# Kernel tuning notes

Hardware: AMD Instinct MI355X
Metric: run time of the kernel (lower is better)

## Reference

```python
import jax, jax.numpy as jnp
import numpy as np

D_MODEL = 1024
N_HEADS = 16
D_HEAD = D_MODEL // N_HEADS
L_NS = 64
B = 1
L_S_VAL = 4096


def setup_inputs() -> dict:
    key = jax.random.key(0)
    k0, k1, k2, k3 = jax.random.split(key, 4)
    d = D_MODEL
    x = jax.random.normal(k0, (B, L_S_VAL + L_NS, d), dtype=jnp.float32)
    # xavier-uniform-ish scales
    s_qkv = (2.0 / (d + 3 * d)) ** 0.5
    s_out = (2.0 / (d + d)) ** 0.5
    W_S = jax.random.normal(k1, (d, 3 * d), dtype=jnp.float32) * s_qkv
    W_NS = jax.random.normal(k2, (L_NS, d, 3 * d), dtype=jnp.float32) * s_qkv
    W_out = jax.random.normal(k3, (d, d), dtype=jnp.float32) * s_out
    return {"x": x, "W_S": W_S, "W_NS": W_NS, "W_out": W_out,
            "L_S": L_S_VAL, "query_start": 2048}


def reference(x, W_S, W_NS, W_out, L_S, query_start):
    Bsz, L_total, D = x.shape
    H, Dh = N_HEADS, D_HEAD
    L_q = L_S - query_start

    x_S = x[:, :L_S]                    # (B, L_S, D)
    x_NS = x[:, L_S:L_S + L_NS]         # (B, L_NS, D)

    qkv_S = jnp.einsum('bsd,do->bso', x_S, W_S)        # shared projection
    qkv_NS = jnp.einsum('bnd,ndo->bno', x_NS, W_NS)    # per-NS-token projection

    Q_S, K_S, V_S = jnp.split(qkv_S, 3, axis=-1)
    Q_NS, K_NS, V_NS = jnp.split(qkv_NS, 3, axis=-1)

    Q = jnp.concatenate([Q_S[:, query_start:], Q_NS], axis=1)  # (B, L_q+L_NS, D)
    K = jnp.concatenate([K_S, K_NS], axis=1)                    # (B, L_total, D)
    V = jnp.concatenate([V_S, V_NS], axis=1)

    def to_heads(t):
        return t.reshape(Bsz, t.shape[1], H, Dh).transpose(0, 2, 1, 3)

    Qh, Kh, Vh = to_heads(Q), to_heads(K), to_heads(V)

    q_pos = jnp.arange(query_start, L_S + L_NS)  # (L_q+L_NS,)
    k_pos = jnp.arange(L_total)                  # (L_total,)
    causal_mask = q_pos[:, None] < k_pos[None, :]  # True = masked out

    scale = Dh ** -0.5
    scores = jnp.einsum('bhqd,bhkd->bhqk', Qh, Kh) * scale
    scores = jnp.where(causal_mask[None, None], -jnp.inf, scores)
    attn = jax.nn.softmax(scores, axis=-1)
    attn = jnp.nan_to_num(attn)

    out = jnp.einsum('bhqk,bhkd->bhqd', attn, Vh)
    out = out.transpose(0, 2, 1, 3).reshape(Bsz, L_q + L_NS, D)
    return jnp.einsum('bqd,de->bqe', out, W_out)
```

## Files before the change

kernel.cpp:

```cpp
#include <hip/hip_runtime.h>

typedef __attribute__((ext_vector_type(8))) short bf16x8;
typedef __attribute__((ext_vector_type(4))) float f32x4;

#define MFMA_BF16(a,b,c) __builtin_amdgcn_mfma_f32_16x16x32_bf16(a,b,c,0,0,0)

#define H_ 16
#define DH 64
#define LQ 2112
#define LK 4160
#define QOFF 2048
#define DM 1024
#define NO 3072

__device__ __forceinline__ unsigned short f2bf(float f) {
  union { float f; unsigned u; } v; v.f = f;
  unsigned u = v.u;
  return (unsigned short)((u + 0x7FFFu + ((u >> 16) & 1u)) >> 16);
}

__device__ __forceinline__ void gl_lds16(const unsigned short* g, unsigned short* l) {
  __builtin_amdgcn_global_load_lds(
      (const __attribute__((address_space(1))) unsigned int*)g,
      (__attribute__((address_space(3))) unsigned int*)l,
      16, 0, 0);
}

__global__ __launch_bounds__(256) void cvt_x(const float* __restrict__ x,
                                             unsigned short* __restrict__ xb) {
  int i = blockIdx.x * 256 + threadIdx.x;
  float4 f = ((const float4*)x)[i];
  ushort4 o;
  o.x = f2bf(f.x); o.y = f2bf(f.y); o.z = f2bf(f.z); o.w = f2bf(f.w);
  ((ushort4*)xb)[i] = o;
}

__global__ __launch_bounds__(256) void transp_bf(const float* __restrict__ in,
                                                 unsigned short* __restrict__ out,
                                                 int R, int C) {
  __shared__ float t[32][33];
  int c0 = blockIdx.x * 32, r0 = blockIdx.y * 32;
  #pragma unroll
  for (int i = threadIdx.y; i < 32; i += 8)
    t[i][threadIdx.x] = in[(size_t)(r0 + i) * C + c0 + threadIdx.x];
  __syncthreads();
  #pragma unroll
  for (int i = threadIdx.y; i < 32; i += 8)
    out[(size_t)(c0 + i) * R + r0 + threadIdx.x] = f2bf(t[threadIdx.x][i]);
}

__global__ __launch_bounds__(256) void qkv_ns_k(const float* __restrict__ x,
                                                const float* __restrict__ W_NS,
                                                float* __restrict__ qkvNS) {
  int oc = blockIdx.x, dc = blockIdx.y, n = blockIdx.z;
  __shared__ float xs[256];
  xs[threadIdx.x] = x[(size_t)(4096 + n) * DM + dc * 256 + threadIdx.x];
  __syncthreads();
  int o0 = oc * 1024 + threadIdx.x * 4;
  const float* W = W_NS + ((size_t)n * DM + dc * 256) * NO + o0;
  float a0 = 0.f, a1 = 0.f, a2 = 0.f, a3 = 0.f;
  #pragma unroll 4
  for (int d = 0; d < 256; ++d) {
    float xv = xs[d];
    float4 w = *(const float4*)(W + (size_t)d * NO);
    a0 = fmaf(xv, w.x, a0); a1 = fmaf(xv, w.y, a1);
    a2 = fmaf(xv, w.z, a2); a3 = fmaf(xv, w.w, a3);
  }
  float* dst = qkvNS + (size_t)n * NO + o0;
  atomicAdd(dst + 0, a0); atomicAdd(dst + 1, a1);
  atomicAdd(dst + 2, a2); atomicAdd(dst + 3, a3);
}

__global__ __launch_bounds__(256) void scatter_ns(const float* __restrict__ qkvNS,
                                                  unsigned short* __restrict__ Qb,
                                                  unsigned short* __restrict__ Kb,
                                                  unsigned short* __restrict__ VbT) {
  int i = blockIdx.x * 256 + threadIdx.x;
  int n = i / NO, o = i - n * NO;
  float v = qkvNS[i];
  int h = (o & 1023) >> 6, dh = o & 63;
  if (o < 1024)       Qb[((size_t)h * LQ + 2048 + n) * DH + dh] = f2bf(v * 0.125f);
  else if (o < 2048)  Kb[((size_t)h * LK + 4096 + n) * DH + dh] = f2bf(v);
  else                VbT[((size_t)(h * 64 + dh)) * LK + 4096 + n] = f2bf(v);
}

__global__ __launch_bounds__(256) void gemm_qkv(const unsigned short* __restrict__ A,
                                                const unsigned short* __restrict__ BT,
                                                unsigned short* __restrict__ Qb,
                                                unsigned short* __restrict__ Kb,
                                                unsigned short* __restrict__ VbT) {
  __shared__ unsigned short At[128 * 32];
  __shared__ unsigned short Bt[128 * 32];
  int tm = blockIdx.x * 128, tn = blockIdx.y * 128;
  int tid = threadIdx.x, wave = tid >> 6, lane = tid & 63;
  int col = lane & 15, quad = lane >> 4;
  int wr = (wave & 1) * 64, wc = (wave >> 1) * 64;
  int srow = tid >> 2, spart = (tid & 3) * 8;

  f32x4 acc[4][4] = {};

  for (int kb = 0; kb < DM; kb += 32) {
    __syncthreads();
    gl_lds16(&A[(size_t)(tm + srow) * DM + kb + spart],       &At[wave * 512]);
    gl_lds16(&A[(size_t)(tm + srow + 64) * DM + kb + spart],  &At[2048 + wave * 512]);
    gl_lds16(&BT[(size_t)(tn + srow) * DM + kb + spart],      &Bt[wave * 512]);
    gl_lds16(&BT[(size_t)(tn + srow + 64) * DM + kb + spart], &Bt[2048 + wave * 512]);
    __syncthreads();
    bf16x8 af[4], bfr[4];
    #pragma unroll
    for (int i = 0; i < 4; ++i) {
      af[i]  = *(const bf16x8*)&At[(wr + i * 16 + col) * 32 + quad * 8];
      bfr[i] = *(const bf16x8*)&Bt[(wc + i * 16 + col) * 32 + quad * 8];
    }
    #pragma unroll
    for (int i = 0; i < 4; ++i)
      #pragma unroll
      for (int j = 0; j < 4; ++j)
        acc[i][j] = MFMA_BF16(af[i], bfr[j], acc[i][j]);
  }

  if (tn >= 2048) {
    #pragma unroll
    for (int i = 0; i < 4; ++i)
      #pragma unroll
      for (int j = 0; j < 4; ++j) {
        int n = tn + wc + j * 16 + col;
        int h = (n & 1023) >> 6, dh = n & 63;
        int m0 = tm + wr + i * 16 + quad * 4;
        ushort4 o;
        o.x = f2bf(acc[i][j][0]); o.y = f2bf(acc[i][j][1]);
        o.z = f2bf(acc[i][j][2]); o.w = f2bf(acc[i][j][3]);
        *(ushort4*)&VbT[((size_t)(h * 64 + dh)) * LK + m0] = o;
      }
  } else if (tn >= 1024) {
    #pragma unroll
    for (int i = 0; i < 4; ++i)
      #pragma unroll
      for (int j = 0; j < 4; ++j)
        #pragma unroll
        for (int r = 0; r < 4; ++r) {
          int m = tm + wr + i * 16 + quad * 4 + r;
          int n = tn + wc + j * 16 + col;
          int h = (n & 1023) >> 6, dh = n & 63;
          Kb[((size_t)h * LK + m) * DH + dh] = f2bf(acc[i][j][r]);
        }
  } else {
    #pragma unroll
    for (int i = 0; i < 4; ++i)
      #pragma unroll
      for (int j = 0; j < 4; ++j)
        #pragma unroll
        for (int r = 0; r < 4; ++r) {
          int m = tm + wr + i * 16 + quad * 4 + r;
          int n = tn + wc + j * 16 + col;
          int h = (n & 1023) >> 6, dh = n & 63;
          if (m >= QOFF) Qb[((size_t)h * LQ + (m - QOFF)) * DH + dh] = f2bf(acc[i][j][r] * 0.125f);
        }
  }
}

__global__ __launch_bounds__(256) void attn(const unsigned short* __restrict__ Qb,
                                            const unsigned short* __restrict__ Kb,
                                            const unsigned short* __restrict__ VbT,
                                            unsigned short* __restrict__ Ob) {
  __shared__ unsigned short Kt[2][64 * 64];
  __shared__ unsigned short Vt[2][64 * 64];
  __shared__ unsigned short Pt[4][16 * 72];
  int h = blockIdx.y;
  int qb = blockIdx.x * 64;
  int tid = threadIdx.x, wave = tid >> 6, lane = tid & 63;
  int col = lane & 15, quad = lane >> 4;
  const unsigned short* Qh = Qb + (size_t)h * LQ * DH;
  const unsigned short* Kh = Kb + (size_t)h * LK * DH;
  const unsigned short* Vh = VbT + (size_t)h * 64 * LK;

  int qrow = qb + wave * 16 + col;
  bf16x8 aq0 = *(const bf16x8*)&Qh[qrow * DH + quad * 8];
  bf16x8 aq1 = *(const bf16x8*)&Qh[qrow * DH + 32 + quad * 8];

  f32x4 oacc[4] = {};
  float m_i[4] = {-3e38f, -3e38f, -3e38f, -3e38f};
  float l_i[4] = {0.f, 0.f, 0.f, 0.f};

  int row0 = tid >> 3;
  int sc8  = ((tid & 7) ^ (row0 & 7)) * 8;
  int xs   = col & 7;

#define STAGE(b, kb_) do { \
    gl_lds16(&Kh[(size_t)((kb_) + row0) * DH + sc8],        &Kt[b][wave * 512]); \
    gl_lds16(&Kh[(size_t)((kb_) + row0 + 32) * DH + sc8],   &Kt[b][2048 + wave * 512]); \
    gl_lds16(&Vh[(size_t)row0 * LK + (kb_) + sc8],          &Vt[b][wave * 512]); \
    gl_lds16(&Vh[(size_t)(row0 + 32) * LK + (kb_) + sc8],   &Vt[b][2048 + wave * 512]); \
  } while (0)

  int nkt = 33 + blockIdx.x;
  STAGE(0, 0);
  int cur = 0;
  for (int kt = 0; kt < nkt; ++kt) {
    int kb = kt << 6;
    __syncthreads();
    if (kt + 1 < nkt) STAGE(cur ^ 1, (kt + 1) << 6);

    const unsigned short* K_ = Kt[cur];
    const unsigned short* V_ = Vt[cur];

    f32x4 s[4] = {};
    #pragma unroll
    for (int f = 0; f < 4; ++f) {
      int krow = (f * 16 + col) * 64;
      bf16x8 b0 = *(const bf16x8*)&K_[krow + (quad ^ xs) * 8];
      bf16x8 b1 = *(const bf16x8*)&K_[krow + (((4 + quad) ^ xs)) * 8];
      s[f] = MFMA_BF16(aq0, b0, s[f]);
      s[f] = MFMA_BF16(aq1, b1, s[f]);
    }

    float alpha[4];
    bool lastt = (kt == nkt - 1);
    #pragma unroll
    for (int r = 0; r < 4; ++r) {
      float v0 = s[0][r], v1 = s[1][r], v2 = s[2][r], v3 = s[3][r];
      if (lastt) {
        int kmax = QOFF + qb + wave * 16 + quad * 4 + r;
        v0 = (kb + col      <= kmax) ? v0 : -3e38f;
        v1 = (kb + 16 + col <= kmax) ? v1 : -3e38f;
        v2 = (kb + 32 + col <= kmax) ? v2 : -3e38f;
        v3 = (kb + 48 + col <= kmax) ? v3 : -3e38f;
      }
      float t = fmaxf(fmaxf(v0, v1), fmaxf(v2, v3));
      t = fmaxf(t, __shfl_xor(t, 1));
      t = fmaxf(t, __shfl_xor(t, 2));
      t = fmaxf(t, __shfl_xor(t, 4));
      t = fmaxf(t, __shfl_xor(t, 8));
      float mn = fmaxf(m_i[r], t);
      alpha[r] = __expf(m_i[r] - mn);
      m_i[r] = mn;
      float e0 = __expf(v0 - mn), e1 = __expf(v1 - mn);
      float e2 = __expf(v2 - mn), e3 = __expf(v3 - mn);
      float su = (e0 + e1) + (e2 + e3);
      su += __shfl_xor(su, 1);
      su += __shfl_xor(su, 2);
      su += __shfl_xor(su, 4);
      su += __shfl_xor(su, 8);
      l_i[r] = l_i[r] * alpha[r] + su;
      int pr = (quad * 4 + r) * 72;
      Pt[wave][pr + col]      = f2bf(e0);
      Pt[wave][pr + 16 + col] = f2bf(e1);
      Pt[wave][pr + 32 + col] = f2bf(e2);
      Pt[wave][pr + 48 + col] = f2bf(e3);
    }
    #pragma unroll
    for (int dt = 0; dt < 4; ++dt)
      #pragma unroll
      for (int r = 0; r < 4; ++r) oacc[dt][r] *= alpha[r];

    asm volatile("s_waitcnt lgkmcnt(0)" ::: "memory");
    bf16x8 ap0 = *(const bf16x8*)&Pt[wave][col * 72 + quad * 8];
    bf16x8 ap1 = *(const bf16x8*)&Pt[wave][col * 72 + 32 + quad * 8];
    #pragma unroll
    for (int dt = 0; dt < 4; ++dt) {
      int dr = (dt * 16 + col) * 64;
      bf16x8 bv0 = *(const bf16x8*)&V_[dr + (quad ^ xs) * 8];
      bf16x8 bv1 = *(const bf16x8*)&V_[dr + (((4 + quad) ^ xs)) * 8];
      oacc[dt] = MFMA_BF16(ap0, bv0, oacc[dt]);
      oacc[dt] = MFMA_BF16(ap1, bv1, oacc[dt]);
    }
    cur ^= 1;
  }
#undef STAGE

  #pragma unroll
  for (int r = 0; r < 4; ++r) {
    int q = qb + wave * 16 + quad * 4 + r;
    float inv = 1.0f / l_i[r];
    #pragma unroll
    for (int dt = 0; dt < 4; ++dt)
      Ob[(size_t)q * DM + h * DH + dt * 16 + col] = f2bf(oacc[dt][r] * inv);
  }
}

__global__ __launch_bounds__(256) void gemm_out_k(const unsigned short* __restrict__ A,
                                                  const unsigned short* __restrict__ BT,
                                                  float* __restrict__ C) {
  __shared__ unsigned short At[128 * 32];
  __shared__ unsigned short Bt[128 * 32];
  int tm = blockIdx.x * 128, tn = blockIdx.y * 128;
  int tid = threadIdx.x, wave = tid >> 6, lane = tid & 63;
  int col = lane & 15, quad = lane >> 4;
  int wr = (wave & 1) * 64, wc = (wave >> 1) * 64;
  int srow = tid >> 2, spart = (tid & 3) * 8;
  int ar0 = min(tm + srow, LQ - 1);
  int ar1 = min(tm + srow + 64, LQ - 1);

  f32x4 acc[4][4] = {};

  for (int kb = 0; kb < DM; kb += 32) {
    __syncthreads();
    gl_lds16(&A[(size_t)ar0 * DM + kb + spart],               &At[wave * 512]);
    gl_lds16(&A[(size_t)ar1 * DM + kb + spart],               &At[2048 + wave * 512]);
    gl_lds16(&BT[(size_t)(tn + srow) * DM + kb + spart],      &Bt[wave * 512]);
    gl_lds16(&BT[(size_t)(tn + srow + 64) * DM + kb + spart], &Bt[2048 + wave * 512]);
    __syncthreads();
    bf16x8 af[4], bfr[4];
    #pragma unroll
    for (int i = 0; i < 4; ++i) {
      af[i]  = *(const bf16x8*)&At[(wr + i * 16 + col) * 32 + quad * 8];
      bfr[i] = *(const bf16x8*)&Bt[(wc + i * 16 + col) * 32 + quad * 8];
    }
    #pragma unroll
    for (int i = 0; i < 4; ++i)
      #pragma unroll
      for (int j = 0; j < 4; ++j)
        acc[i][j] = MFMA_BF16(af[i], bfr[j], acc[i][j]);
  }

  #pragma unroll
  for (int i = 0; i < 4; ++i)
    #pragma unroll
    for (int j = 0; j < 4; ++j)
      #pragma unroll
      for (int r = 0; r < 4; ++r) {
        int m = tm + wr + i * 16 + quad * 4 + r;
        int n = tn + wc + j * 16 + col;
        if (m < LQ) C[(size_t)m * DM + n] = acc[i][j][r];
      }
}

extern "C" void kernel_launch(void* const* d_in, const int* in_sizes, int n_in,
                              void* d_out, int out_size, void* d_ws, size_t ws_size,
                              hipStream_t stream) {
  const float* x     = (const float*)d_in[0];
  const float* W_S   = (const float*)d_in[1];
  const float* W_NS  = (const float*)d_in[2];
  const float* W_out = (const float*)d_in[3];
  char* ws = (char*)d_ws;

  unsigned short* xb    = (unsigned short*)(ws + 0);
  unsigned short* WST   = (unsigned short*)(ws + 8519680);
  unsigned short* WOT   = (unsigned short*)(ws + 14811136);
  float*          qkvNS = (float*)(ws + 16908288);
  unsigned short* Qb    = (unsigned short*)(ws + 17694720);
  unsigned short* Kb    = (unsigned short*)(ws + 22020096);
  unsigned short* VbT   = (unsigned short*)(ws + 30539776);
  unsigned short* Ob    = (unsigned short*)(ws + 39059456);
  float* out = (float*)d_out;

  hipMemsetAsync(qkvNS, 0, 64 * NO * sizeof(float), stream);
  cvt_x<<<4160, 256, 0, stream>>>(x, xb);
  transp_bf<<<dim3(96, 32), dim3(32, 8), 0, stream>>>(W_S, WST, 1024, 3072);
  transp_bf<<<dim3(32, 32), dim3(32, 8), 0, stream>>>(W_out, WOT, 1024, 1024);
  qkv_ns_k<<<dim3(3, 4, 64), 256, 0, stream>>>(x, W_NS, qkvNS);
  scatter_ns<<<768, 256, 0, stream>>>(qkvNS, Qb, Kb, VbT);
  gemm_qkv<<<dim3(32, 24), 256, 0, stream>>>(xb, WST, Qb, Kb, VbT);
  attn<<<dim3(33, 16), 256, 0, stream>>>(Qb, Kb, VbT, Ob);
  gemm_out_k<<<dim3(17, 8), 256, 0, stream>>>(Ob, WOT, out);
}
```

Baseline: 1.274 ms.

## Fuse prep kernels, merge NS projection into QKV GEMM, reorder attention blocks

Merges the x conversion and both weight transposes into one prep launch. The per-NS-token projection now runs inside the QKV GEMM grid, interleaved with the GEMM tiles, which removes the memset, atomics and scatter kernel. Attention launches the longest query blocks first, folds log2(e) into the Q scale so it can use exp2f, and raises wave priority around the MFMA sections. This cuts launch count and tail imbalance, but the NS blocks each stream a full weight slice serially and may become stragglers in the GEMM grid.

```diff
diff --git a/kernel.cpp b/kernel.cpp
--- a/kernel.cpp
+++ b/kernel.cpp
@@ -12,6 +12,7 @@
 #define QOFF 2048
 #define DM 1024
 #define NO 3072
+#define QSCALE 0.1803368801f
 
 __device__ __forceinline__ unsigned short f2bf(float f) {
   union { float f; unsigned u; } v; v.f = f;
@@ -26,73 +27,77 @@
       16, 0, 0);
 }
 
-__global__ __launch_bounds__(256) void cvt_x(const float* __restrict__ x,
-                                             unsigned short* __restrict__ xb) {
-  int i = blockIdx.x * 256 + threadIdx.x;
-  float4 f = ((const float4*)x)[i];
-  ushort4 o;
-  o.x = f2bf(f.x); o.y = f2bf(f.y); o.z = f2bf(f.z); o.w = f2bf(f.w);
-  ((ushort4*)xb)[i] = o;
-}
-
-__global__ __launch_bounds__(256) void transp_bf(const float* __restrict__ in,
-                                                 unsigned short* __restrict__ out,
-                                                 int R, int C) {
+__global__ __launch_bounds__(256) void prep(const float* __restrict__ x,
+                                            const float* __restrict__ W_S,
+                                            const float* __restrict__ W_out,
+                                            unsigned short* __restrict__ xb,
+                                            unsigned short* __restrict__ WST,
+                                            unsigned short* __restrict__ WOT) {
+  int idx = blockIdx.x, tid = threadIdx.x;
+  if (idx < 4160) {
+    int i = idx * 256 + tid;
+    float4 f = ((const float4*)x)[i];
+    ushort4 o;
+    o.x = f2bf(f.x); o.y = f2bf(f.y); o.z = f2bf(f.z); o.w = f2bf(f.w);
+    ((ushort4*)xb)[i] = o;
+    return;
+  }
   __shared__ float t[32][33];
-  int c0 = blockIdx.x * 32, r0 = blockIdx.y * 32;
+  const float* in; unsigned short* out; int C, bx, by;
+  if (idx < 7232) { int r = idx - 4160; bx = r % 96; by = r / 96; in = W_S;   out = WST; C = 3072; }
+  else            { int r = idx - 7232; bx = r % 32; by = r / 32; in = W_out; out = WOT; C = 1024; }
+  int c0 = bx * 32, r0 = by * 32;
+  int tx = tid & 31, ty = tid >> 5;
   #pragma unroll
-  for (int i = threadIdx.y; i < 32; i += 8)
-    t[i][threadIdx.x] = in[(size_t)(r0 + i) * C + c0 + threadIdx.x];
+  for (int i = ty; i < 32; i += 8)
+    t[i][tx] = in[(size_t)(r0 + i) * C + c0 + tx];
   __syncthreads();
   #pragma unroll
-  for (int i = threadIdx.y; i < 32; i += 8)
-    out[(size_t)(c0 + i) * R + r0 + threadIdx.x] = f2bf(t[threadIdx.x][i]);
-}
-
-__global__ __launch_bounds__(256) void qkv_ns_k(const float* __restrict__ x,
-                                                const float* __restrict__ W_NS,
-                                                float* __restrict__ qkvNS) {
-  int oc = blockIdx.x, dc = blockIdx.y, n = blockIdx.z;
-  __shared__ float xs[256];
-  xs[threadIdx.x] = x[(size_t)(4096 + n) * DM + dc * 256 + threadIdx.x];
-  __syncthreads();
-  int o0 = oc * 1024 + threadIdx.x * 4;
-  const float* W = W_NS + ((size_t)n * DM + dc * 256) * NO + o0;
-  float a0 = 0.f, a1 = 0.f, a2 = 0.f, a3 = 0.f;
-  #pragma unroll 4
-  for (int d = 0; d < 256; ++d) {
-    float xv = xs[d];
-    float4 w = *(const float4*)(W + (size_t)d * NO);
-    a0 = fmaf(xv, w.x, a0); a1 = fmaf(xv, w.y, a1);
-    a2 = fmaf(xv, w.z, a2); a3 = fmaf(xv, w.w, a3);
-  }
-  float* dst = qkvNS + (size_t)n * NO + o0;
-  atomicAdd(dst + 0, a0); atomicAdd(dst + 1, a1);
-  atomicAdd(dst + 2, a2); atomicAdd(dst + 3, a3);
-}
-
-__global__ __launch_bounds__(256) void scatter_ns(const float* __restrict__ qkvNS,
-                                                  unsigned short* __restrict__ Qb,
-                                                  unsigned short* __restrict__ Kb,
-                                                  unsigned short* __restrict__ VbT) {
-  int i = blockIdx.x * 256 + threadIdx.x;
-  int n = i / NO, o = i - n * NO;
-  float v = qkvNS[i];
-  int h = (o & 1023) >> 6, dh = o & 63;
-  if (o < 1024)       Qb[((size_t)h * LQ + 2048 + n) * DH + dh] = f2bf(v * 0.125f);
-  else if (o < 2048)  Kb[((size_t)h * LK + 4096 + n) * DH + dh] = f2bf(v);
-  else                VbT[((size_t)(h * 64 + dh)) * LK + 4096 + n] = f2bf(v);
-}
-
-__global__ __launch_bounds__(256) void gemm_qkv(const unsigned short* __restrict__ A,
-                                                const unsigned short* __restrict__ BT,
-                                                unsigned short* __restrict__ Qb,
-                                                unsigned short* __restrict__ Kb,
-                                                unsigned short* __restrict__ VbT) {
+  for (int i = ty; i < 32; i += 8)
+    out[(size_t)(c0 + i) * 1024 + r0 + tx] = f2bf(t[tx][i]);
+}
+
+__global__ __launch_bounds__(256) void fused_qkv(const unsigned short* __restrict__ A,
+                                                 const unsigned short* __restrict__ BT,
+                                                 const float* __restrict__ x,
+                                                 const float* __restrict__ W_NS,
+                                                 unsigned short* __restrict__ Qb,
+                                                 unsigned short* __restrict__ Kb,
+                                                 unsigned short* __restrict__ VbT) {
+  int idx = blockIdx.x, tid = threadIdx.x;
+
+  if (idx % 3 == 2) {
+    __shared__ float xs[1024];
+    int nid = idx / 3;
+    int oc2 = nid % 6, n = nid / 6;
+    ((float4*)xs)[tid] = ((const float4*)(x + (size_t)(4096 + n) * DM))[tid];
+    __syncthreads();
+    int o0 = oc2 * 512 + tid * 2;
+    const float* W = W_NS + (size_t)n * DM * NO + o0;
+    float a0 = 0.f, a1 = 0.f;
+    #pragma unroll 8
+    for (int d = 0; d < DM; ++d) {
+      float xv = xs[d];
+      float2 w = *(const float2*)(W + (size_t)d * NO);
+      a0 = fmaf(xv, w.x, a0); a1 = fmaf(xv, w.y, a1);
+    }
+    #pragma unroll
+    for (int j = 0; j < 2; ++j) {
+      int o = o0 + j;
+      float v = j ? a1 : a0;
+      int h = (o & 1023) >> 6, dh = o & 63;
+      if (o < 1024)       Qb[((size_t)h * LQ + 2048 + n) * DH + dh] = f2bf(v * QSCALE);
+      else if (o < 2048)  Kb[((size_t)h * LK + 4096 + n) * DH + dh] = f2bf(v);
+      else                VbT[((size_t)(h * 64 + dh)) * LK + 4096 + n] = f2bf(v);
+    }
+    return;
+  }
+
   __shared__ unsigned short At[128 * 32];
   __shared__ unsigned short Bt[128 * 32];
-  int tm = blockIdx.x * 128, tn = blockIdx.y * 128;
-  int tid = threadIdx.x, wave = tid >> 6, lane = tid & 63;
+  int g = (idx / 3) * 2 + (idx % 3);
+  int tm = (g & 31) * 128, tn = (g >> 5) * 128;
+  int wave = tid >> 6, lane = tid & 63;
   int col = lane & 15, quad = lane >> 4;
   int wr = (wave & 1) * 64, wc = (wave >> 1) * 64;
   int srow = tid >> 2, spart = (tid & 3) * 8;
@@ -154,7 +159,7 @@
           int m = tm + wr + i * 16 + quad * 4 + r;
           int n = tn + wc + j * 16 + col;
           int h = (n & 1023) >> 6, dh = n & 63;
-          if (m >= QOFF) Qb[((size_t)h * LQ + (m - QOFF)) * DH + dh] = f2bf(acc[i][j][r] * 0.125f);
+          if (m >= QOFF) Qb[((size_t)h * LQ + (m - QOFF)) * DH + dh] = f2bf(acc[i][j][r] * QSCALE);
         }
   }
 }
@@ -167,7 +172,8 @@
   __shared__ unsigned short Vt[2][64 * 64];
   __shared__ unsigned short Pt[4][16 * 72];
   int h = blockIdx.y;
-  int qb = blockIdx.x * 64;
+  int qi = 32 - (int)blockIdx.x;
+  int qb = qi * 64;
   int tid = threadIdx.x, wave = tid >> 6, lane = tid & 63;
   int col = lane & 15, quad = lane >> 4;
   const unsigned short* Qh = Qb + (size_t)h * LQ * DH;
@@ -193,7 +199,7 @@
     gl_lds16(&Vh[(size_t)(row0 + 32) * LK + (kb_) + sc8],   &Vt[b][2048 + wave * 512]); \
   } while (0)
 
-  int nkt = 33 + blockIdx.x;
+  int nkt = 33 + qi;
   STAGE(0, 0);
   int cur = 0;
   for (int kt = 0; kt < nkt; ++kt) {
@@ -205,6 +211,7 @@
     const unsigned short* V_ = Vt[cur];
 
     f32x4 s[4] = {};
+    __builtin_amdgcn_s_setprio(1);
     #pragma unroll
     for (int f = 0; f < 4; ++f) {
       int krow = (f * 16 + col) * 64;
@@ -213,6 +220,7 @@
       s[f] = MFMA_BF16(aq0, b0, s[f]);
       s[f] = MFMA_BF16(aq1, b1, s[f]);
     }
+    __builtin_amdgcn_s_setprio(0);
 
     float alpha[4];
     bool lastt = (kt == nkt - 1);
@@ -232,10 +240,10 @@
       t = fmaxf(t, __shfl_xor(t, 4));
       t = fmaxf(t, __shfl_xor(t, 8));
       float mn = fmaxf(m_i[r], t);
-      alpha[r] = __expf(m_i[r] - mn);
+      alpha[r] = exp2f(m_i[r] - mn);
       m_i[r] = mn;
-      float e0 = __expf(v0 - mn), e1 = __expf(v1 - mn);
-      float e2 = __expf(v2 - mn), e3 = __expf(v3 - mn);
+      float e0 = exp2f(v0 - mn), e1 = exp2f(v1 - mn);
+      float e2 = exp2f(v2 - mn), e3 = exp2f(v3 - mn);
       float su = (e0 + e1) + (e2 + e3);
       su += __shfl_xor(su, 1);
       su += __shfl_xor(su, 2);
@@ -256,6 +264,7 @@
     asm volatile("s_waitcnt lgkmcnt(0)" ::: "memory");
     bf16x8 ap0 = *(const bf16x8*)&Pt[wave][col * 72 + quad * 8];
     bf16x8 ap1 = *(const bf16x8*)&Pt[wave][col * 72 + 32 + quad * 8];
+    __builtin_amdgcn_s_setprio(1);
     #pragma unroll
     for (int dt = 0; dt < 4; ++dt) {
       int dr = (dt * 16 + col) * 64;
@@ -264,6 +273,7 @@
       oacc[dt] = MFMA_BF16(ap0, bv0, oacc[dt]);
       oacc[dt] = MFMA_BF16(ap1, bv1, oacc[dt]);
     }
+    __builtin_amdgcn_s_setprio(0);
     cur ^= 1;
   }
 #undef STAGE
@@ -337,20 +347,14 @@
   unsigned short* xb    = (unsigned short*)(ws + 0);
   unsigned short* WST   = (unsigned short*)(ws + 8519680);
   unsigned short* WOT   = (unsigned short*)(ws + 14811136);
-  float*          qkvNS = (float*)(ws + 16908288);
   unsigned short* Qb    = (unsigned short*)(ws + 17694720);
   unsigned short* Kb    = (unsigned short*)(ws + 22020096);
   unsigned short* VbT   = (unsigned short*)(ws + 30539776);
   unsigned short* Ob    = (unsigned short*)(ws + 39059456);
   float* out = (float*)d_out;
 
-  hipMemsetAsync(qkvNS, 0, 64 * NO * sizeof(float), stream);
-  cvt_x<<<4160, 256, 0, stream>>>(x, xb);
-  transp_bf<<<dim3(96, 32), dim3(32, 8), 0, stream>>>(W_S, WST, 1024, 3072);
-  transp_bf<<<dim3(32, 32), dim3(32, 8), 0, stream>>>(W_out, WOT, 1024, 1024);
-  qkv_ns_k<<<dim3(3, 4, 64), 256, 0, stream>>>(x, W_NS, qkvNS);
-  scatter_ns<<<768, 256, 0, stream>>>(qkvNS, Qb, Kb, VbT);
-  gemm_qkv<<<dim3(32, 24), 256, 0, stream>>>(xb, WST, Qb, Kb, VbT);
+  prep<<<8256, 256, 0, stream>>>(x, W_S, W_out, xb, WST, WOT);
+  fused_qkv<<<1152, 256, 0, stream>>>(xb, WST, x, W_NS, Qb, Kb, VbT);
   attn<<<dim3(33, 16), 256, 0, stream>>>(Qb, Kb, VbT, Ob);
   gemm_out_k<<<dim3(17, 8), 256, 0, stream>>>(Ob, WOT, out);
 }
```

New measurement: 1.263 ms. Within noise of the previous version (-0.8%).
